# Kernel tuning notes

Measured on AMD Instinct MI355X. Metric: run time of the kernel, lower is better.

The kernel has to match this reference:

```python
import jax, jax.numpy as jnp
import numpy as np

MEMORY_SLOTS = 256
MEMORY_TOPK = 8
RETRIEVAL_WEIGHT = 0.5


def setup_inputs() -> dict:
    key = jax.random.key(0)
    ks = jax.random.split(key, 5)
    B, T, C = 8, 2048, 1024
    scale = 1.0 / np.sqrt(C)
    return {
        "x": jax.random.normal(ks[0], (B, T, C), dtype=jnp.float32),
        "Wq": jax.random.normal(ks[1], (C, C), dtype=jnp.float32) * scale,
        "Wk": jax.random.normal(ks[2], (C, C), dtype=jnp.float32) * scale,
        "Wv": jax.random.normal(ks[3], (C, C), dtype=jnp.float32) * scale,
        "Wp": jax.random.normal(ks[4], (C, C), dtype=jnp.float32) * scale,
    }


def reference(x, Wq, Wk, Wv, Wp):
    B, T, C = x.shape
    num_slots = min(T, MEMORY_SLOTS)
    topk = min(num_slots, MEMORY_TOPK)
    # adaptive_avg_pool1d with T divisible by num_slots == mean over equal chunks
    slots = x.reshape(B, num_slots, T // num_slots, C).mean(axis=2)  # [B,S,C]
    # Linear layers (torch: x @ W.T, no bias)
    q = jnp.einsum("btc,dc->btd", x, Wq)        # [B,T,C]
    k = jnp.einsum("bsc,dc->bsd", slots, Wk)    # [B,S,C]
    v = jnp.einsum("bsc,dc->bsd", slots, Wv)    # [B,S,C]
    scores = jnp.einsum("btd,bsd->bts", q, k) * (1.0 / jnp.sqrt(jnp.float32(C)))
    topk_scores, topk_indices = jax.lax.top_k(scores, topk)  # [B,T,K]
    topk_weights = jax.nn.softmax(topk_scores, axis=-1)       # [B,T,K]
    # gather selected value rows: [B,T,K,C]
    retrieved = jnp.take_along_axis(v[:, None, :, :], topk_indices[..., None], axis=2)
    retrieved = jnp.einsum("btkc,btk->btc", retrieved, topk_weights)
    out = jnp.einsum("btc,dc->btd", retrieved, Wp) * RETRIEVAL_WEIGHT
    return out
```

## Files before the change

### kernel.cpp

```cpp
#include <hip/hip_runtime.h>
#include <cstdint>
#include <cstddef>

#define Tt 2048
#define Cc 1024
#define Ss 256

using short8 = __attribute__((ext_vector_type(8))) short;
using f32x4  = __attribute__((ext_vector_type(4))) float;
typedef const __attribute__((address_space(1))) void* as1_cvp;
typedef __attribute__((address_space(3))) void* as3_vp;

__device__ __forceinline__ unsigned short f2bf(float f) {
  unsigned int u = __float_as_uint(f);
  u += 0x7fffu + ((u >> 16) & 1u);
  return (unsigned short)(u >> 16);
}
__device__ __forceinline__ float bf2f(unsigned short h) {
  return __uint_as_float(((unsigned)h) << 16);
}
__device__ __forceinline__ void split3(float v, unsigned short& h, unsigned short& m, unsigned short& l) {
  h = f2bf(v);
  float r = v - bf2f(h);
  m = f2bf(r);
  l = f2bf(r - bf2f(m));
}

__device__ __forceinline__ int sw32(int row, int q) {
  return row * 32 + ((q ^ ((row >> 1) & 3)) << 3);
}

__global__ __launch_bounds__(256) void poolsplit_k(const float* __restrict__ x, unsigned short* __restrict__ sp) {
  const long PS2 = 2048l * 1024;
  const int sli = blockIdx.x;
  const int c = threadIdx.x << 2;
  const float* src = x + (size_t)sli * 8 * Cc + c;
  float a[4] = {0.f, 0.f, 0.f, 0.f};
#pragma unroll
  for (int j = 0; j < 8; j++) {
    float4 v = *(const float4*)(src + (size_t)j * Cc);
    a[0] += v.x; a[1] += v.y; a[2] += v.z; a[3] += v.w;
  }
  unsigned short h[4], m[4], l[4];
#pragma unroll
  for (int e = 0; e < 4; e++) split3(a[e] * 0.125f, h[e], m[e], l[e]);
  size_t o = (size_t)sli * Cc + c;
  *(uint2*)&sp[o]           = uint2{(unsigned)h[0] | ((unsigned)h[1] << 16), (unsigned)h[2] | ((unsigned)h[3] << 16)};
  *(uint2*)&sp[o + PS2]     = uint2{(unsigned)m[0] | ((unsigned)m[1] << 16), (unsigned)m[2] | ((unsigned)m[3] << 16)};
  *(uint2*)&sp[o + 2 * PS2] = uint2{(unsigned)l[0] | ((unsigned)l[1] << 16), (unsigned)l[2] | ((unsigned)l[3] << 16)};
}

__global__ __launch_bounds__(256) void split_t_k(const float* __restrict__ src, unsigned short* __restrict__ dst,
                                                 long pstride, int npl) {
  __shared__ unsigned short th[64][68], tm[64][68], tl[64][68];
  const int r0 = blockIdx.y << 6, c0 = blockIdx.x << 6;
  const int tid = threadIdx.x;
#pragma unroll
  for (int p = 0; p < 4; p++) {
    int r = (p << 4) + (tid >> 4);
    int c = (tid & 15) << 2;
    float4 v = *(const float4*)&src[(size_t)(r0 + r) * Cc + c0 + c];
    unsigned short h, m, l;
    split3(v.x, h, m, l); th[c + 0][r] = h; tm[c + 0][r] = m; tl[c + 0][r] = l;
    split3(v.y, h, m, l); th[c + 1][r] = h; tm[c + 1][r] = m; tl[c + 1][r] = l;
    split3(v.z, h, m, l); th[c + 2][r] = h; tm[c + 2][r] = m; tl[c + 2][r] = l;
    split3(v.w, h, m, l); th[c + 3][r] = h; tm[c + 3][r] = m; tl[c + 3][r] = l;
  }
  __syncthreads();
#pragma unroll
  for (int p = 0; p < 4; p++) {
    int r = (p << 4) + (tid >> 4);
    int c = (tid & 15) << 2;
    size_t o = (size_t)(c0 + r) * Cc + r0 + c;
    *(uint2*)&dst[o] = uint2{(unsigned)th[r][c] | ((unsigned)th[r][c+1] << 16),
                             (unsigned)th[r][c+2] | ((unsigned)th[r][c+3] << 16)};
    *(uint2*)&dst[o + pstride] = uint2{(unsigned)tm[r][c] | ((unsigned)tm[r][c+1] << 16),
                                       (unsigned)tm[r][c+2] | ((unsigned)tm[r][c+3] << 16)};
    if (npl == 3)
      *(uint2*)&dst[o + 2 * pstride] = uint2{(unsigned)tl[r][c] | ((unsigned)tl[r][c+1] << 16),
                                             (unsigned)tl[r][c+2] | ((unsigned)tl[r][c+3] << 16)};
  }
}

__global__ __launch_bounds__(256) void split_k(const float* __restrict__ src, unsigned short* __restrict__ dst,
                                               long pstride, int npl) {
  int id = blockIdx.x * 256 + threadIdx.x;
  int c = id << 2;
  float4 v = *(const float4*)&src[c];
  unsigned short h[4], m[4], l[4];
  split3(v.x, h[0], m[0], l[0]); split3(v.y, h[1], m[1], l[1]);
  split3(v.z, h[2], m[2], l[2]); split3(v.w, h[3], m[3], l[3]);
  *(uint2*)&dst[c] = uint2{(unsigned)h[0] | ((unsigned)h[1] << 16), (unsigned)h[2] | ((unsigned)h[3] << 16)};
  *(uint2*)&dst[c + pstride] = uint2{(unsigned)m[0] | ((unsigned)m[1] << 16), (unsigned)m[2] | ((unsigned)m[3] << 16)};
  if (npl == 3)
    *(uint2*)&dst[c + 2 * pstride] = uint2{(unsigned)l[0] | ((unsigned)l[1] << 16), (unsigned)l[2] | ((unsigned)l[3] << 16)};
}

template<int NT, int SPLIT_OUT>
__device__ __forceinline__ void gemm3_body(unsigned short* LDS,
                                           const unsigned short* __restrict__ Ap, long apl,
                                           const unsigned short* __restrict__ Bp, long bpl,
                                           float* __restrict__ C,
                                           unsigned short* __restrict__ Cs, long cpl,
                                           float scale) {
  constexpr int NPL = (NT == 6) ? 3 : 2;
  constexpr int BUFS = 2 * NPL * 2048;
  const int tid = threadIdx.x, lane = tid & 63, wid = tid >> 6;
  const int m0 = blockIdx.y << 6, n0 = blockIdx.x << 6;

  const unsigned short* sp[2 * NPL];
  int dof[2 * NPL];
#pragma unroll
  for (int i = 0; i < 2 * NPL; i++) {
    int s = wid * 2 * NPL + i;
    int tile = s >> 2;
    int ci = ((s & 3) << 6) | lane;
    int row = ci >> 2;
    int q = (ci & 3) ^ ((row >> 1) & 3);
    int isB = tile >= NPL;
    int pl = isB ? tile - NPL : tile;
    const unsigned short* base = isB ? (Bp + (size_t)pl * bpl) : (Ap + (size_t)pl * apl);
    int r0 = isB ? n0 : m0;
    sp[i] = base + (size_t)(r0 + row) * Cc + (q << 3);
    dof[i] = (tile * 2048 + ((s & 3) << 9)) * 2;
  }

  const int wm = (wid >> 1) << 5, wn = (wid & 1) << 5;
  const int lm = lane & 15, lq = lane >> 4;
  constexpr int PA[6] = {0, 0, 1, 0, 2, 1};
  constexpr int PB[6] = {0, 1, 0, 2, 0, 1};
  const f32x4 zero = {0.f, 0.f, 0.f, 0.f};
  f32x4 acc[2][2] = {{zero, zero}, {zero, zero}};

#pragma unroll
  for (int i = 0; i < 2 * NPL; i++) {
    __builtin_amdgcn_global_load_lds((as1_cvp)sp[i], (as3_vp)((char*)LDS + dof[i]), 16, 0, 0);
    sp[i] += 32;
  }
  __syncthreads();

  int cur = 0;
  for (int k0 = 0; k0 < Cc; k0 += 32) {
    if (k0 + 32 < Cc) {
      const int nb = (cur ^ 1) * (BUFS * 2);
#pragma unroll
      for (int i = 0; i < 2 * NPL; i++) {
        __builtin_amdgcn_global_load_lds((as1_cvp)sp[i], (as3_vp)((char*)LDS + nb + dof[i]), 16, 0, 0);
        sp[i] += 32;
      }
    }
    const int cb = cur * BUFS;
    short8 af[2][NPL], bf[2][NPL];
#pragma unroll
    for (int i = 0; i < 2; i++)
#pragma unroll
      for (int p = 0; p < NPL; p++) {
        af[i][p] = *(const short8*)&LDS[cb + p * 2048 + sw32(wm + (i << 4) + lm, lq)];
        bf[i][p] = *(const short8*)&LDS[cb + (NPL + p) * 2048 + sw32(wn + (i << 4) + lm, lq)];
      }
#pragma unroll
    for (int i = 0; i < 2; i++)
#pragma unroll
      for (int j = 0; j < 2; j++)
#pragma unroll
        for (int t = 0; t < NT; t++)
          acc[i][j] = __builtin_amdgcn_mfma_f32_16x16x32_bf16(af[i][PA[t]], bf[j][PB[t]], acc[i][j], 0, 0, 0);
    __syncthreads();
    cur ^= 1;
  }
#pragma unroll
  for (int i = 0; i < 2; i++)
#pragma unroll
    for (int j = 0; j < 2; j++)
#pragma unroll
      for (int r = 0; r < 4; r++) {
        int gr = m0 + wm + (i << 4) + (lq << 2) + r;
        int gc = n0 + wn + (j << 4) + lm;
        size_t o = (size_t)gr * Cc + gc;
        float v = acc[i][j][r] * scale;
        if (SPLIT_OUT) {
          unsigned short h = f2bf(v);
          float rr = v - bf2f(h);
          unsigned short mm2 = f2bf(rr);
          Cs[o] = h;
          Cs[o + cpl] = mm2;
          if (NPL == 3) Cs[o + 2 * (size_t)cpl] = f2bf(rr - bf2f(mm2));
        } else {
          C[o] = v;
        }
      }
}

template<int NT, int SPLIT_OUT>
__device__ __forceinline__ void gemm128_body(unsigned short* LDS,
                                             const unsigned short* __restrict__ Ap, long apl,
                                             const unsigned short* __restrict__ Bp, long bpl,
                                             float* __restrict__ C,
                                             unsigned short* __restrict__ Cs, long cpl,
                                             float scale) {
  constexpr int NPL = (NT == 6) ? 3 : 2;
  constexpr int BUFS = 2 * NPL * 4096;
  const int tid = threadIdx.x, lane = tid & 63, wid = tid >> 6;
  const int m0 = blockIdx.y << 7, n0 = blockIdx.x << 7;

  const unsigned short* sp[4 * NPL];
  int dof[4 * NPL];
#pragma unroll
  for (int i = 0; i < 4 * NPL; i++) {
    int s = wid * 4 * NPL + i;
    int tile = s >> 3;
    int ci = ((s & 7) << 6) | lane;
    int row = ci >> 2;
    int q = (ci & 3) ^ ((row >> 1) & 3);
    int isB = tile >= NPL;
    int pl = isB ? tile - NPL : tile;
    const unsigned short* base = isB ? (Bp + (size_t)pl * bpl) : (Ap + (size_t)pl * apl);
    int r0 = isB ? n0 : m0;
    sp[i] = base + (size_t)(r0 + row) * Cc + (q << 3);
    dof[i] = (tile * 4096 + ((s & 7) << 9)) * 2;
  }

  const int wr = (wid >> 1) << 6, wc = (wid & 1) << 6;
  const int lm = lane & 15, lq = lane >> 4;
  constexpr int PA[6] = {0, 0, 1, 0, 2, 1};
  constexpr int PB[6] = {0, 1, 0, 2, 0, 1};
  const f32x4 zero = {0.f, 0.f, 0.f, 0.f};
  f32x4 acc[4][4];
#pragma unroll
  for (int i = 0; i < 4; i++)
#pragma unroll
    for (int j = 0; j < 4; j++) acc[i][j] = zero;

#pragma unroll
  for (int i = 0; i < 4 * NPL; i++) {
    __builtin_amdgcn_global_load_lds((as1_cvp)sp[i], (as3_vp)((char*)LDS + dof[i]), 16, 0, 0);
    sp[i] += 32;
  }
  __syncthreads();

  int cur = 0;
  for (int k0 = 0; k0 < Cc; k0 += 32) {
    if (k0 + 32 < Cc) {
      const int nb = (cur ^ 1) * (BUFS * 2);
#pragma unroll
      for (int i = 0; i < 4 * NPL; i++) {
        __builtin_amdgcn_global_load_lds((as1_cvp)sp[i], (as3_vp)((char*)LDS + nb + dof[i]), 16, 0, 0);
        sp[i] += 32;
      }
    }
    const int cb = cur * BUFS;
    short8 af[4][NPL];
#pragma unroll
    for (int i = 0; i < 4; i++)
#pragma unroll
      for (int p = 0; p < NPL; p++)
        af[i][p] = *(const short8*)&LDS[cb + p * 4096 + sw32(wr + (i << 4) + lm, lq)];
#pragma unroll
    for (int j = 0; j < 4; j++) {
      short8 bf[NPL];
#pragma unroll
      for (int p = 0; p < NPL; p++)
        bf[p] = *(const short8*)&LDS[cb + (NPL + p) * 4096 + sw32(wc + (j << 4) + lm, lq)];
#pragma unroll
      for (int i = 0; i < 4; i++)
#pragma unroll
        for (int t = 0; t < NT; t++)
          acc[i][j] = __builtin_amdgcn_mfma_f32_16x16x32_bf16(af[i][PA[t]], bf[PB[t]], acc[i][j], 0, 0, 0);
    }
    __syncthreads();
    cur ^= 1;
  }
#pragma unroll
  for (int i = 0; i < 4; i++)
#pragma unroll
    for (int j = 0; j < 4; j++)
#pragma unroll
      for (int r = 0; r < 4; r++) {
        int gr = m0 + wr + (i << 4) + (lq << 2) + r;
        int gc = n0 + wc + (j << 4) + lm;
        size_t o = (size_t)gr * Cc + gc;
        float v = acc[i][j][r] * scale;
        if (SPLIT_OUT) {
          unsigned short h = f2bf(v);
          float rr = v - bf2f(h);
          unsigned short mm2 = f2bf(rr);
          Cs[o] = h;
          Cs[o + cpl] = mm2;
          if (NPL == 3) Cs[o + 2 * (size_t)cpl] = f2bf(rr - bf2f(mm2));
        } else {
          C[o] = v;
        }
      }
}

__global__ __launch_bounds__(256) void gemm35_k(const unsigned short* __restrict__ Wqt,
                                                const unsigned short* __restrict__ Wkt,
                                                const unsigned short* __restrict__ Wpp,
                                                const unsigned short* __restrict__ Wvt,
                                                unsigned short* __restrict__ MtT,
                                                unsigned short* __restrict__ W2p, long ps1) {
  __shared__ unsigned short LDS[24576];
  if (blockIdx.z == 0)
    gemm3_body<6, 1>(LDS, Wqt, ps1, Wkt, ps1, nullptr, MtT, ps1, 1.0f);
  else
    gemm3_body<3, 1>(LDS, Wpp, ps1, Wvt, ps1, nullptr, W2p, ps1, 1.0f);
}

__global__ __launch_bounds__(256) void gemm46_k(const unsigned short* __restrict__ slotp, long ps2,
                                                const unsigned short* __restrict__ MtT,
                                                const unsigned short* __restrict__ W2p, long ps1,
                                                unsigned short* __restrict__ kqp,
                                                float* __restrict__ u) {
  __shared__ unsigned short LDS[49152];
  if (blockIdx.z == 0)
    gemm128_body<6, 1>(LDS, slotp, ps2, MtT, ps1, nullptr, kqp, ps2, 1.0f);
  else
    gemm128_body<3, 0>(LDS, slotp, ps2, W2p, ps1, u, nullptr, 0, 1.0f);
}

__global__ __launch_bounds__(512) void scores_topk_k(const float* __restrict__ x,
                                                     const unsigned short* __restrict__ kqp,
                                                     float* __restrict__ topw, int* __restrict__ topi) {
  __shared__ __align__(16) char smem[125952];
  unsigned short* lds16 = (unsigned short*)smem;
  float* sc = (float*)smem;

  const int tid = threadIdx.x, lane = tid & 63, wid = tid >> 6;
  const int bid = blockIdx.x;
  const int b = bid & 7, tt = bid >> 3;

  const char* ksrc[6];
  int kdst[6];
#pragma unroll
  for (int i = 0; i < 6; i++) {
    int s = wid * 6 + i;
    int p = s >> 4, sub = s & 15;
    int ci = (sub << 6) | lane;
    int row = ci >> 2;
    int q = (ci & 3) ^ ((row >> 1) & 3);
    ksrc[i] = (const char*)(kqp + (size_t)p * (2048l * 1024) + ((size_t)b * Ss + row) * Cc + (q << 3));
    kdst[i] = p * 16384 + sub * 1024;
  }
  const int spr = tid >> 3, spk = (tid & 7) << 2;
  const float* xsrc = x + ((size_t)b * Tt + (size_t)tt * 64 + spr) * Cc + spk;

  const int wm = (wid & 1) << 5;
  const int wn = (wid >> 1) << 6;
  const int lm = lane & 15, lq = lane >> 4;
  const int XP = 49152;

  constexpr int PA[6] = {0, 0, 1, 0, 2, 1};
  constexpr int PB[6] = {0, 1, 0, 2, 0, 1};
  const f32x4 zero = {0.f, 0.f, 0.f, 0.f};
  f32x4 acc[2][4];
#pragma unroll
  for (int i = 0; i < 2; i++)
#pragma unroll
    for (int j = 0; j < 4; j++) acc[i][j] = zero;

  {
    float4 xv = *(const float4*)xsrc; xsrc += 32;
#pragma unroll
    for (int i = 0; i < 6; i++) {
      __builtin_amdgcn_global_load_lds((as1_cvp)ksrc[i], (as3_vp)(smem + kdst[i]), 16, 0, 0);
      ksrc[i] += 64;
    }
    unsigned short h[4], m[4], l[4];
    split3(xv.x, h[0], m[0], l[0]); split3(xv.y, h[1], m[1], l[1]);
    split3(xv.z, h[2], m[2], l[2]); split3(xv.w, h[3], m[3], l[3]);
    int o = XP + spr * 36 + spk;
    *(uint2*)&lds16[o]        = uint2{(unsigned)h[0] | ((unsigned)h[1] << 16), (unsigned)h[2] | ((unsigned)h[3] << 16)};
    *(uint2*)&lds16[o + 2304] = uint2{(unsigned)m[0] | ((unsigned)m[1] << 16), (unsigned)m[2] | ((unsigned)m[3] << 16)};
    *(uint2*)&lds16[o + 4608] = uint2{(unsigned)l[0] | ((unsigned)l[1] << 16), (unsigned)l[2] | ((unsigned)l[3] << 16)};
  }
  __syncthreads();

  int cur = 0;
  for (int ks = 0; ks < 32; ks++) {
    const int nb = cur ^ 1;
    float4 xv2;
    if (ks < 31) {
      xv2 = *(const float4*)xsrc; xsrc += 32;
#pragma unroll
      for (int i = 0; i < 6; i++) {
        __builtin_amdgcn_global_load_lds((as1_cvp)ksrc[i], (as3_vp)(smem + nb * 49152 + kdst[i]), 16, 0, 0);
        ksrc[i] += 64;
      }
    }
    const int xb = XP + cur * 6912;
    const int kb = cur * 24576;
    short8 afr[2][3], bfr[4][3];
#pragma unroll
    for (int i = 0; i < 2; i++)
#pragma unroll
      for (int p = 0; p < 3; p++)
        afr[i][p] = *(const short8*)&lds16[xb + p * 2304 + (wm + (i << 4) + lm) * 36 + (lq << 3)];
#pragma unroll
    for (int j = 0; j < 4; j++) {
      int br = wn + (j << 4) + lm;
      int bo = (br << 5) + ((lq ^ ((br >> 1) & 3)) << 3);
#pragma unroll
      for (int p = 0; p < 3; p++)
        bfr[j][p] = *(const short8*)&lds16[kb + p * 8192 + bo];
    }
#pragma unroll
    for (int i = 0; i < 2; i++)
#pragma unroll
      for (int j = 0; j < 4; j++)
#pragma unroll
        for (int t = 0; t < 6; t++)
          acc[i][j] = __builtin_amdgcn_mfma_f32_16x16x32_bf16(afr[i][PA[t]], bfr[j][PB[t]], acc[i][j], 0, 0, 0);
    if (ks < 31) {
      unsigned short h[4], m[4], l[4];
      split3(xv2.x, h[0], m[0], l[0]); split3(xv2.y, h[1], m[1], l[1]);
      split3(xv2.z, h[2], m[2], l[2]); split3(xv2.w, h[3], m[3], l[3]);
      int o = XP + nb * 6912 + spr * 36 + spk;
      *(uint2*)&lds16[o]        = uint2{(unsigned)h[0] | ((unsigned)h[1] << 16), (unsigned)h[2] | ((unsigned)h[3] << 16)};
      *(uint2*)&lds16[o + 2304] = uint2{(unsigned)m[0] | ((unsigned)m[1] << 16), (unsigned)m[2] | ((unsigned)m[3] << 16)};
      *(uint2*)&lds16[o + 4608] = uint2{(unsigned)l[0] | ((unsigned)l[1] << 16), (unsigned)l[2] | ((unsigned)l[3] << 16)};
    }
    __syncthreads();
    cur ^= 1;
  }

#pragma unroll
  for (int i = 0; i < 2; i++)
#pragma unroll
    for (int j = 0; j < 4; j++)
#pragma unroll
      for (int r = 0; r < 4; r++)
        sc[(wm + (i << 4) + (lq << 2) + r) * 260 + wn + (j << 4) + lm] = acc[i][j][r] * 0.03125f;
  __syncthreads();

  for (int r2 = 0; r2 < 8; r2++) {
    int row = (wid << 3) + r2;
    float4 v = *(const float4*)(sc + row * 260 + (lane << 2));
    float cand[4] = {v.x, v.y, v.z, v.w};
    float topv[8]; int tops[8];
#pragma unroll
    for (int k = 0; k < 8; k++) {
      float bv = -1e30f; int bs = 1 << 20;
#pragma unroll
      for (int e = 0; e < 4; e++) {
        int s = (lane << 2) + e;
        if (cand[e] > bv || (cand[e] == bv && s < bs)) { bv = cand[e]; bs = s; }
      }
#pragma unroll
      for (int m = 32; m >= 1; m >>= 1) {
        float ov = __shfl_xor(bv, m, 64);
        int   os = __shfl_xor(bs, m, 64);
        if (ov > bv || (ov == bv && os < bs)) { bv = ov; bs = os; }
      }
      topv[k] = bv; tops[k] = bs;
      if ((bs >> 2) == lane) cand[bs & 3] = -1e30f;
    }
    float mx = topv[0];
    float sum = 0.f;
#pragma unroll
    for (int k = 0; k < 8; k++) sum += expf(topv[k] - mx);
    if (lane < 8) {
      float myv = topv[0]; int myi = tops[0];
#pragma unroll
      for (int k = 1; k < 8; k++) if (lane == k) { myv = topv[k]; myi = tops[k]; }
      size_t trow = (size_t)b * Tt + (size_t)tt * 64 + row;
      topw[trow * 8 + lane] = expf(myv - mx) / sum;
      topi[trow * 8 + lane] = myi;
    }
  }
}

__global__ __launch_bounds__(256) void gatherout_k(const float* __restrict__ u, const float* __restrict__ topw,
                                                   const int* __restrict__ topi, float* __restrict__ out) {
  __shared__ float w[8];
  __shared__ int  id8[8];
  const int row = blockIdx.x;
  const int b = row >> 11;
  if (threadIdx.x < 8) {
    w[threadIdx.x]   = topw[(size_t)row * 8 + threadIdx.x];
    id8[threadIdx.x] = topi[(size_t)row * 8 + threadIdx.x];
  }
  __syncthreads();
  int c = threadIdx.x << 2;
  float ax = 0.f, ay = 0.f, az = 0.f, aw = 0.f;
#pragma unroll
  for (int j = 0; j < 8; j++) {
    const float4 vv = *(const float4*)&u[((size_t)(b << 8) + id8[j]) * Cc + c];
    float wj = w[j];
    ax = fmaf(wj, vv.x, ax); ay = fmaf(wj, vv.y, ay);
    az = fmaf(wj, vv.z, az); aw = fmaf(wj, vv.w, aw);
  }
  *(float4*)&out[(size_t)row * Cc + c] = make_float4(ax * 0.5f, ay * 0.5f, az * 0.5f, aw * 0.5f);
}

extern "C" void kernel_launch(void* const* d_in, const int* in_sizes, int n_in,
                              void* d_out, int out_size, void* d_ws, size_t ws_size,
                              hipStream_t stream) {
  (void)in_sizes; (void)n_in; (void)out_size; (void)ws_size;
  const float* x  = (const float*)d_in[0];
  const float* Wq = (const float*)d_in[1];
  const float* Wk = (const float*)d_in[2];
  const float* Wv = (const float*)d_in[3];
  const float* Wp = (const float*)d_in[4];
  float* out = (float*)d_out;

  char* ws = (char*)d_ws;
  const size_t MB = 1ull << 20;
  const long PS1 = 1024l * 1024;
  const long PS2 = 2048l * 1024;
  unsigned short* slotp = (unsigned short*)(ws + 0 * MB);
  unsigned short* Wqt   = (unsigned short*)(ws + 12 * MB);
  unsigned short* Wkt   = (unsigned short*)(ws + 18 * MB);
  unsigned short* Wvt   = (unsigned short*)(ws + 24 * MB);
  unsigned short* Wpp   = (unsigned short*)(ws + 28 * MB);
  unsigned short* MtT   = (unsigned short*)(ws + 32 * MB);
  unsigned short* kqp   = (unsigned short*)(ws + 38 * MB);
  unsigned short* W2p   = (unsigned short*)(ws + 50 * MB);
  float*          u     = (float*)(ws + 54 * MB);
  float*          topw  = (float*)(ws + 62 * MB);
  int*            topi  = (int*)(ws + 62 * MB + 512 * 1024);

  poolsplit_k<<<2048, 256, 0, stream>>>(x, slotp);
  split_t_k<<<dim3(16, 16), 256, 0, stream>>>(Wq, Wqt, PS1, 3);
  split_t_k<<<dim3(16, 16), 256, 0, stream>>>(Wk, Wkt, PS1, 3);
  split_t_k<<<dim3(16, 16), 256, 0, stream>>>(Wv, Wvt, PS1, 2);
  split_k<<<1024, 256, 0, stream>>>(Wp, Wpp, PS1, 2);
  gemm35_k<<<dim3(16, 16, 2), 256, 0, stream>>>(Wqt, Wkt, Wpp, Wvt, MtT, W2p, PS1);
  gemm46_k<<<dim3(8, 16, 2), 256, 0, stream>>>(slotp, PS2, MtT, W2p, PS1, kqp, u);
  scores_topk_k<<<256, 512, 0, stream>>>(x, kqp, topw, topi);
  gatherout_k<<<16384, 256, 0, stream>>>(u, topw, topi, out);
}
```

Before: 361.9 us.

## Split 6-term kq GEMM across two z-slices, merge split transposes, reorder gather rows

The 6-product bf16x3 GEMM that produces kq is divided into two 3-product halves, each running as a separate z-slice of gemm46 and writing fp32 partial results. A new kqsplit kernel adds the two halves and performs the hi/mid/lo split. This balances gemm46's z-slices and lowers its LDS footprint, at the cost of an extra kernel and extra fp32 traffic. The three Wq/Wk/Wv transpose-split launches are also merged into a single launch, and gatherout's block-to-row mapping is interleaved across batches.

Result: no change. 360.0 us (-0.5%).

```diff
diff --git a/kernel.cpp b/kernel.cpp
--- a/kernel.cpp
+++ b/kernel.cpp
@@ -50,9 +50,15 @@
   *(uint2*)&sp[o + 2 * PS2] = uint2{(unsigned)l[0] | ((unsigned)l[1] << 16), (unsigned)l[2] | ((unsigned)l[3] << 16)};
 }
 
-__global__ __launch_bounds__(256) void split_t_k(const float* __restrict__ src, unsigned short* __restrict__ dst,
-                                                 long pstride, int npl) {
+__global__ __launch_bounds__(256) void split_t3_k(const float* __restrict__ Wq, const float* __restrict__ Wk,
+                                                  const float* __restrict__ Wv,
+                                                  unsigned short* __restrict__ Wqt, unsigned short* __restrict__ Wkt,
+                                                  unsigned short* __restrict__ Wvt, long pstride) {
   __shared__ unsigned short th[64][68], tm[64][68], tl[64][68];
+  const int z = blockIdx.z;
+  const float* src = (z == 0) ? Wq : (z == 1) ? Wk : Wv;
+  unsigned short* dst = (z == 0) ? Wqt : (z == 1) ? Wkt : Wvt;
+  const int npl = (z == 2) ? 2 : 3;
   const int r0 = blockIdx.y << 6, c0 = blockIdx.x << 6;
   const int tid = threadIdx.x;
 #pragma unroll
@@ -94,6 +100,22 @@
   *(uint2*)&dst[c + pstride] = uint2{(unsigned)m[0] | ((unsigned)m[1] << 16), (unsigned)m[2] | ((unsigned)m[3] << 16)};
   if (npl == 3)
     *(uint2*)&dst[c + 2 * pstride] = uint2{(unsigned)l[0] | ((unsigned)l[1] << 16), (unsigned)l[2] | ((unsigned)l[3] << 16)};
+}
+
+__global__ __launch_bounds__(256) void kqsplit_k(const float* __restrict__ a, const float* __restrict__ bsrc,
+                                                 unsigned short* __restrict__ dst) {
+  const long PS2 = 2048l * 1024;
+  int id = blockIdx.x * 256 + threadIdx.x;
+  int c = id << 2;
+  float4 va = *(const float4*)&a[c];
+  float4 vb = *(const float4*)&bsrc[c];
+  float s0 = va.x + vb.x, s1 = va.y + vb.y, s2 = va.z + vb.z, s3 = va.w + vb.w;
+  unsigned short h[4], m[4], l[4];
+  split3(s0, h[0], m[0], l[0]); split3(s1, h[1], m[1], l[1]);
+  split3(s2, h[2], m[2], l[2]); split3(s3, h[3], m[3], l[3]);
+  *(uint2*)&dst[c]           = uint2{(unsigned)h[0] | ((unsigned)h[1] << 16), (unsigned)h[2] | ((unsigned)h[3] << 16)};
+  *(uint2*)&dst[c + PS2]     = uint2{(unsigned)m[0] | ((unsigned)m[1] << 16), (unsigned)m[2] | ((unsigned)m[3] << 16)};
+  *(uint2*)&dst[c + 2 * PS2] = uint2{(unsigned)l[0] | ((unsigned)l[1] << 16), (unsigned)l[2] | ((unsigned)l[3] << 16)};
 }
 
 template<int NT, int SPLIT_OUT>
@@ -191,7 +213,7 @@
       }
 }
 
-template<int NT, int SPLIT_OUT>
+template<int NT, int SPLIT_OUT, int ALT>
 __device__ __forceinline__ void gemm128_body(unsigned short* LDS,
                                              const unsigned short* __restrict__ Ap, long apl,
                                              const unsigned short* __restrict__ Bp, long bpl,
@@ -222,8 +244,8 @@
 
   const int wr = (wid >> 1) << 6, wc = (wid & 1) << 6;
   const int lm = lane & 15, lq = lane >> 4;
-  constexpr int PA[6] = {0, 0, 1, 0, 2, 1};
-  constexpr int PB[6] = {0, 1, 0, 2, 0, 1};
+  constexpr int PAt[2][6] = {{0, 0, 1, 0, 2, 1}, {0, 1, 1, 0, 0, 0}};
+  constexpr int PBt[2][6] = {{0, 1, 0, 2, 0, 1}, {1, 0, 1, 0, 0, 0}};
   const f32x4 zero = {0.f, 0.f, 0.f, 0.f};
   f32x4 acc[4][4];
 #pragma unroll
@@ -265,7 +287,7 @@
       for (int i = 0; i < 4; i++)
 #pragma unroll
         for (int t = 0; t < NT; t++)
-          acc[i][j] = __builtin_amdgcn_mfma_f32_16x16x32_bf16(af[i][PA[t]], bf[PB[t]], acc[i][j], 0, 0, 0);
+          acc[i][j] = __builtin_amdgcn_mfma_f32_16x16x32_bf16(af[i][PAt[ALT][t]], bf[PBt[ALT][t]], acc[i][j], 0, 0, 0);
     }
     __syncthreads();
     cur ^= 1;
@@ -309,13 +331,15 @@
 __global__ __launch_bounds__(256) void gemm46_k(const unsigned short* __restrict__ slotp, long ps2,
                                                 const unsigned short* __restrict__ MtT,
                                                 const unsigned short* __restrict__ W2p, long ps1,
-                                                unsigned short* __restrict__ kqp,
+                                                float* __restrict__ kqfA, float* __restrict__ kqfB,
                                                 float* __restrict__ u) {
-  __shared__ unsigned short LDS[49152];
+  __shared__ unsigned short LDS[32768];
   if (blockIdx.z == 0)
-    gemm128_body<6, 1>(LDS, slotp, ps2, MtT, ps1, nullptr, kqp, ps2, 1.0f);
+    gemm128_body<3, 0, 0>(LDS, slotp, 2 * ps2, MtT, 2 * ps1, kqfA, nullptr, 0, 1.0f);
+  else if (blockIdx.z == 1)
+    gemm128_body<3, 0, 1>(LDS, slotp, ps2, MtT, ps1, kqfB, nullptr, 0, 1.0f);
   else
-    gemm128_body<3, 0>(LDS, slotp, ps2, W2p, ps1, u, nullptr, 0, 1.0f);
+    gemm128_body<3, 0, 0>(LDS, slotp, ps2, W2p, ps1, u, nullptr, 0, 1.0f);
 }
 
 __global__ __launch_bounds__(512) void scores_topk_k(const float* __restrict__ x,
@@ -473,8 +497,9 @@
                                                    const int* __restrict__ topi, float* __restrict__ out) {
   __shared__ float w[8];
   __shared__ int  id8[8];
-  const int row = blockIdx.x;
-  const int b = row >> 11;
+  const int bid = blockIdx.x;
+  const int row = ((bid & 7) << 11) | (bid >> 3);
+  const int b = bid & 7;
   if (threadIdx.x < 8) {
     w[threadIdx.x]   = topw[(size_t)row * 8 + threadIdx.x];
     id8[threadIdx.x] = topi[(size_t)row * 8 + threadIdx.x];
@@ -518,14 +543,15 @@
   float*          u     = (float*)(ws + 54 * MB);
   float*          topw  = (float*)(ws + 62 * MB);
   int*            topi  = (int*)(ws + 62 * MB + 512 * 1024);
+  float*          kqfA  = (float*)(ws + 63 * MB);
+  float*          kqfB  = (float*)(ws + 71 * MB);
 
   poolsplit_k<<<2048, 256, 0, stream>>>(x, slotp);
-  split_t_k<<<dim3(16, 16), 256, 0, stream>>>(Wq, Wqt, PS1, 3);
-  split_t_k<<<dim3(16, 16), 256, 0, stream>>>(Wk, Wkt, PS1, 3);
-  split_t_k<<<dim3(16, 16), 256, 0, stream>>>(Wv, Wvt, PS1, 2);
+  split_t3_k<<<dim3(16, 16, 3), 256, 0, stream>>>(Wq, Wk, Wv, Wqt, Wkt, Wvt, PS1);
   split_k<<<1024, 256, 0, stream>>>(Wp, Wpp, PS1, 2);
   gemm35_k<<<dim3(16, 16, 2), 256, 0, stream>>>(Wqt, Wkt, Wpp, Wvt, MtT, W2p, PS1);
-  gemm46_k<<<dim3(8, 16, 2), 256, 0, stream>>>(slotp, PS2, MtT, W2p, PS1, kqp, u);
+  gemm46_k<<<dim3(8, 16, 3), 256, 0, stream>>>(slotp, PS2, MtT, W2p, PS1, kqfA, kqfB, u);
+  kqsplit_k<<<2048, 256, 0, stream>>>(kqfA, kqfB, kqp);
   scores_topk_k<<<256, 512, 0, stream>>>(x, kqp, topw, topi);
   gatherout_k<<<16384, 256, 0, stream>>>(u, topw, topi, out);
 }
```
